# Optimization experiments

Measured on AMD Instinct MI355X. Metric: run time of the kernel, lower is better.

The kernel has to match this reference:

```python
import jax, jax.numpy as jnp
import numpy as np

PROTO_DIM = 512
PROTO_NUM = 4096
BSZ = 256
SUBTEXT_NUM = 64
TEMP = 0.9


def setup_inputs() -> dict:
    key = jax.random.key(0)
    k1, k2, k3 = jax.random.split(key, 3)
    subtexts = jax.random.normal(k1, (BSZ, SUBTEXT_NUM, PROTO_DIM), dtype=jnp.float32)
    prototype = jax.random.normal(k2, (PROTO_NUM, PROTO_DIM), dtype=jnp.float32)
    uniform = jax.random.uniform(k3, (BSZ * SUBTEXT_NUM, PROTO_NUM), dtype=jnp.float32)
    return {"subtexts": subtexts, "prototype": prototype, "uniform": uniform}


def reference(subtexts, prototype, uniform):
    # flatten: [N, D] with N = bsz * subtext_num
    flatten = subtexts.reshape(-1, PROTO_DIM)
    # dist: [N, proto_num] = flatten @ prototype.T
    dist = jnp.einsum("nd,pd->np", flatten, prototype)
    # Gumbel noise g = -log(-log(u)), matching torch F.gumbel_softmax sampling
    tiny = jnp.float32(1e-10)
    gumbel = -jnp.log(-jnp.log(uniform + tiny) + tiny)
    # noisy logits -> softmax over codebook dim (tau = curr_temp)
    soft_one_hot = jax.nn.softmax((dist + gumbel) / jnp.float32(TEMP), axis=1)
    # output: [N, D] soft codebook lookup
    output = jnp.einsum("np,pd->nd", soft_one_hot, prototype)
    proto_idx = jnp.argmax(soft_one_hot, axis=1)
    proto_loss = jnp.mean(jnp.abs(output - flatten))
    return (output, proto_loss, proto_idx)
```

## Files before the change

kernel.cpp:

```cpp
#include <hip/hip_runtime.h>
#include <math.h>

#define NROWS 16384
#define DIM   512
#define NPROTO 4096
#define TINV (1.0f / 0.9f)
#define LOSS_OFF ((size_t)NROWS * DIM)
#define IDX_OFF  ((size_t)NROWS * DIM + 1)

typedef __attribute__((ext_vector_type(8))) short short8;
typedef __attribute__((ext_vector_type(4))) float f32x4;

__global__ void zero_loss_kernel(float* out) { out[LOSS_OFF] = 0.0f; }

static __device__ __forceinline__ unsigned short f2bf(float x) {
    unsigned u = __float_as_uint(x);
    u = (u + 0x7fffu + ((u >> 16) & 1u)) >> 16;
    return (unsigned short)u;
}
static __device__ __forceinline__ float bf2f(unsigned short b) {
    return __uint_as_float(((unsigned)b) << 16);
}
static __device__ __forceinline__ void gl_lds16(const void* g, void* l) {
    __builtin_amdgcn_global_load_lds((const __attribute__((address_space(1))) unsigned int*)g,
                                     (__attribute__((address_space(3))) unsigned int*)l, 16, 0, 0);
}

__global__ __launch_bounds__(256)
void split_bf16_kernel(const float* __restrict__ src, unsigned short* __restrict__ dhi,
                       unsigned short* __restrict__ dmid, int nrows)
{
    __shared__ __align__(16) unsigned short shi[64][520];
    __shared__ __align__(16) unsigned short smid[64][520];
    const int tid = threadIdx.x;
    const int r0 = blockIdx.x * 64;
#pragma unroll
    for (int q = 0; q < 32; ++q) {
        int idx = q * 256 + tid;
        int row = idx >> 7;
        int k4 = (idx & 127) << 2;
        float4 v = *(const float4*)&src[(size_t)(r0 + row) * DIM + k4];
        unsigned short h0 = f2bf(v.x), h1 = f2bf(v.y), h2 = f2bf(v.z), h3 = f2bf(v.w);
        shi[row][k4] = h0; shi[row][k4 + 1] = h1; shi[row][k4 + 2] = h2; shi[row][k4 + 3] = h3;
        smid[row][k4]     = f2bf(v.x - bf2f(h0));
        smid[row][k4 + 1] = f2bf(v.y - bf2f(h1));
        smid[row][k4 + 2] = f2bf(v.z - bf2f(h2));
        smid[row][k4 + 3] = f2bf(v.w - bf2f(h3));
    }
    __syncthreads();
    const int row = tid & 63;
#pragma unroll
    for (int i = 0; i < 16; ++i) {
        int c = i * 4 + (tid >> 6);
        size_t o = (size_t)c * nrows + r0 + row;
        ((ulonglong2*)dhi)[o]  = *(const ulonglong2*)&shi[row][c * 8];
        ((ulonglong2*)dmid)[o] = *(const ulonglong2*)&smid[row][c * 8];
    }
}

#define BM 32
#define BN 256
#define NCHUNK (NPROTO / BN)
#define NT 16
#define CAP 80
#define PRUNE_AT 56
#define THRH 12.0f

__global__ __launch_bounds__(256, 2)
void attr_proto_mfma(const float* __restrict__ A, const float* __restrict__ Pr,
                     const float* __restrict__ U, float* __restrict__ out,
                     const unsigned short* __restrict__ wsAhi, const unsigned short* __restrict__ wsAmid,
                     const unsigned short* __restrict__ wsPhi, const unsigned short* __restrict__ wsPmid)
{
    __shared__ __align__(16) unsigned short sA[2][4][BM][8];
    __shared__ __align__(16) unsigned short sP[2][4][BN][8];
    __shared__ float hZ[BM][CAP];
    __shared__ unsigned short hI[BM][CAP];
    __shared__ int cnt[BM];
    __shared__ float mRun[BM], lRun[BM];
    __shared__ float wMax[4][BM], wSum[4][BM];
    __shared__ float epZ[8][BM];
    __shared__ int epI[8][BM];
    __shared__ int pruneFlag;

    const int tid = threadIdx.x;
    const int w = tid >> 6;
    const int lane = tid & 63;
    const int l4 = lane & 15;
    const int lh = lane >> 4;
    const int row0 = blockIdx.x * BM;

    for (int r = tid; r < BM; r += 256) { cnt[r] = 0; mRun[r] = -1e30f; lRun[r] = 0.f; }
    if (tid == 0) pruneFlag = 0;

    const unsigned short* gp[9];
    int str9[9];
    int fx9[9];
    unsigned short* ld9[9];
#pragma unroll
    for (int si = 0; si < 9; ++si) {
        int s = w * 9 + si;
        if (s < 4) {
            int sp = s >> 1, gpair = s & 1;
            int g = gpair * 2 + (lane >> 5);
            gp[si]  = (sp ? wsAmid : wsAhi) + ((size_t)g * NROWS + row0 + (lane & 31)) * 8;
            str9[si] = 4 * NROWS * 8;
            fx9[si]  = -16 * 4 * NROWS * 8;
            ld9[si] = &sA[sp][gpair * 2][0][0] + (size_t)lane * 8;
        } else {
            int p = s - 4;
            int sp = p >> 4, rem = p & 15, g = rem >> 2, q = rem & 3;
            gp[si]  = (sp ? wsPmid : wsPhi) + ((size_t)g * NPROTO + q * 64 + lane) * 8;
            str9[si] = 4 * NPROTO * 8;
            fx9[si]  = -16 * 4 * NPROTO * 8 + BN * 8;
            ld9[si] = &sP[sp][g][q * 64][0] + (size_t)lane * 8;
        }
    }
#define DO_STAGE() { _Pragma("unroll") for (int si = 0; si < 9; ++si) { gl_lds16(gp[si], ld9[si]); gp[si] += str9[si]; } }

    DO_STAGE();
    __syncthreads();

    for (int ch = 0; ch < NCHUNK; ++ch) {
        const int pbase = ch * BN;
        f32x4 acc[2][4];
#pragma unroll
        for (int mf = 0; mf < 2; ++mf)
#pragma unroll
            for (int nf = 0; nf < 4; ++nf) { acc[mf][nf][0]=0.f; acc[mf][nf][1]=0.f; acc[mf][nf][2]=0.f; acc[mf][nf][3]=0.f; }

#pragma unroll 2
        for (int t = 0; t < NT; ++t) {
            if (t > 0) {
                __syncthreads();
                DO_STAGE();
                __syncthreads();
            }
            short8 a[2][2], b[4][2];
#pragma unroll
            for (int mf = 0; mf < 2; ++mf) {
                a[mf][0] = *(const short8*)&sA[0][lh][mf * 16 + l4][0];
                a[mf][1] = *(const short8*)&sA[1][lh][mf * 16 + l4][0];
            }
#pragma unroll
            for (int nf = 0; nf < 4; ++nf) {
                b[nf][0] = *(const short8*)&sP[0][lh][w * 64 + nf * 16 + l4][0];
                b[nf][1] = *(const short8*)&sP[1][lh][w * 64 + nf * 16 + l4][0];
            }
#pragma unroll
            for (int mf = 0; mf < 2; ++mf)
#pragma unroll
                for (int nf = 0; nf < 4; ++nf) {
                    acc[mf][nf] = __builtin_amdgcn_mfma_f32_16x16x32_bf16(a[mf][0], b[nf][0], acc[mf][nf], 0, 0, 0);
                    acc[mf][nf] = __builtin_amdgcn_mfma_f32_16x16x32_bf16(a[mf][0], b[nf][1], acc[mf][nf], 0, 0, 0);
                    acc[mf][nf] = __builtin_amdgcn_mfma_f32_16x16x32_bf16(a[mf][1], b[nf][0], acc[mf][nf], 0, 0, 0);
                }
        }
        __syncthreads();
        if (ch + 1 < NCHUNK) {
#pragma unroll
            for (int si = 0; si < 9; ++si) gp[si] += fx9[si];
            DO_STAGE();
        }

#pragma unroll
        for (int mf = 0; mf < 2; ++mf) {
            float uu[16];
            const int rb = row0 + mf * 16 + lh * 4;
#pragma unroll
            for (int nf = 0; nf < 4; ++nf)
#pragma unroll
                for (int r = 0; r < 4; ++r)
                    uu[nf * 4 + r] = U[(size_t)(rb + r) * NPROTO + pbase + w * 64 + nf * 16 + l4];
#pragma unroll
            for (int nf = 0; nf < 4; ++nf)
#pragma unroll
                for (int r = 0; r < 4; ++r) {
                    float g = -__logf(-__logf(uu[nf * 4 + r] + 1e-10f) + 1e-10f);
                    acc[mf][nf][r] = (acc[mf][nf][r] + g) * TINV;
                }
        }
#pragma unroll
        for (int mf = 0; mf < 2; ++mf) {
            f32x4 rm;
#pragma unroll
            for (int r = 0; r < 4; ++r)
                rm[r] = fmaxf(fmaxf(acc[mf][0][r], acc[mf][1][r]), fmaxf(acc[mf][2][r], acc[mf][3][r]));
#pragma unroll
            for (int off = 1; off < 16; off <<= 1)
#pragma unroll
                for (int r = 0; r < 4; ++r) rm[r] = fmaxf(rm[r], __shfl_xor(rm[r], off));
            if (l4 == 0)
#pragma unroll
                for (int r = 0; r < 4; ++r) wMax[w][mf * 16 + lh * 4 + r] = rm[r];
        }
        __syncthreads();
#pragma unroll
        for (int mf = 0; mf < 2; ++mf) {
#pragma unroll
            for (int r = 0; r < 4; ++r) {
                const int rl = mf * 16 + lh * 4 + r;
                float gm = fmaxf(fmaxf(wMax[0][rl], wMax[1][rl]), fmaxf(wMax[2][rl], wMax[3][rl]));
                float mn = fmaxf(mRun[rl], gm);
                float s = 0.f;
#pragma unroll
                for (int nf = 0; nf < 4; ++nf) s += __expf(acc[mf][nf][r] - mn);
#pragma unroll
                for (int off = 1; off < 16; off <<= 1) s += __shfl_xor(s, off);
                if (l4 == 0) wSum[w][rl] = s;
                float thrv = mn - THRH;
#pragma unroll
                for (int nf = 0; nf < 4; ++nf) {
                    float z = acc[mf][nf][r];
                    if (z > thrv) {
                        int pos = atomicAdd(&cnt[rl], 1);
                        if (pos < CAP) { hZ[rl][pos] = z; hI[rl][pos] = (unsigned short)(pbase + w * 64 + nf * 16 + l4); }
                    }
                }
            }
        }
        __syncthreads();
        if (tid < BM) {
            float gm = fmaxf(fmaxf(wMax[0][tid], wMax[1][tid]), fmaxf(wMax[2][tid], wMax[3][tid]));
            float mn = fmaxf(mRun[tid], gm);
            float S = wSum[0][tid] + wSum[1][tid] + wSum[2][tid] + wSum[3][tid];
            lRun[tid] = lRun[tid] * __expf(mRun[tid] - mn) + S;
            mRun[tid] = mn;
            if (cnt[tid] > PRUNE_AT) atomicOr(&pruneFlag, 1);
        }
        __syncthreads();
        if (pruneFlag) {
            for (int r = 0; r < BM; ++r) {
                int c0 = min(cnt[r], CAP);
                if (c0 > PRUNE_AT) {
                    float thr2 = mRun[r] - THRH;
                    float ez = 0.f; int ei = 0; bool keep = false;
                    if (tid < c0) { ez = hZ[r][tid]; ei = hI[r][tid]; keep = ez > thr2; }
                    __syncthreads();
                    if (tid == 0) cnt[r] = 0;
                    __syncthreads();
                    if (keep) { int pos = atomicAdd(&cnt[r], 1); hZ[r][pos] = ez; hI[r][pos] = (unsigned short)ei; }
                    __syncthreads();
                }
            }
            if (tid == 0) pruneFlag = 0;
        }
        __syncthreads();
    }

    __syncthreads();
    const int rq = tid & 31;
    const int qq = tid >> 5;
    {
        const int c = min(cnt[rq], CAP);
        float qm = -1e30f;
        for (int e = qq; e < c; e += 8) qm = fmaxf(qm, hZ[rq][e]);
        epZ[qq][rq] = qm;
    }
    __syncthreads();
    {
        const int c = min(cnt[rq], CAP);
        float bzr = epZ[0][rq];
#pragma unroll
        for (int q = 1; q < 8; ++q) bzr = fmaxf(bzr, epZ[q][rq]);
        const float win = bzr - 3.0f;
        float bestz = -1e30f; int bestp = 1 << 30;
        const float* ap = &A[(size_t)(row0 + rq) * DIM];
        for (int e = qq; e < c; e += 8) {
            if (hZ[rq][e] > win) {
                const int p = hI[rq][e];
                const float* pp = &Pr[(size_t)p * DIM];
                float d = 0.f;
                for (int k = 0; k < DIM; k += 4) {
                    float4 av = *(const float4*)&ap[k];
                    float4 pv = *(const float4*)&pp[k];
                    d = fmaf(av.x, pv.x, d);
                    d = fmaf(av.y, pv.y, d);
                    d = fmaf(av.z, pv.z, d);
                    d = fmaf(av.w, pv.w, d);
                }
                float u = U[(size_t)(row0 + rq) * NPROTO + p];
                float g = -logf(-logf(u + 1e-10f) + 1e-10f);
                float zz = (d + g) * (1.0f / 0.9f);
                if (zz > bestz || (zz == bestz && p < bestp)) { bestz = zz; bestp = p; }
            }
        }
        __syncthreads();
        epZ[qq][rq] = bestz;
        epI[qq][rq] = bestp;
    }
    __syncthreads();
    if (tid < BM) {
        float bz2 = epZ[0][tid]; int bp2 = epI[0][tid];
#pragma unroll
        for (int q = 1; q < 8; ++q) {
            float z = epZ[q][tid]; int p = epI[q][tid];
            if (z > bz2 || (z == bz2 && p < bp2)) { bz2 = z; bp2 = p; }
        }
        out[IDX_OFF + row0 + tid] = (float)bp2;
    }

    float lossAcc = 0.f;
    for (int r = w; r < BM; r += 4) {
        const int grow = row0 + r;
        const int c = min(cnt[r], CAP);
        const float mm = mRun[r];
        const float li = 1.0f / lRun[r];
        float o[8];
#pragma unroll
        for (int q = 0; q < 8; ++q) o[q] = 0.f;
        for (int e = 0; e < c; ++e) {
            float wgt = __expf(hZ[r][e] - mm) * li;
            const float* pp = &Pr[(size_t)hI[r][e] * DIM + lane * 8];
            float4 p0 = *(const float4*)pp;
            float4 p1 = *(const float4*)(pp + 4);
            o[0] += wgt * p0.x; o[1] += wgt * p0.y; o[2] += wgt * p0.z; o[3] += wgt * p0.w;
            o[4] += wgt * p1.x; o[5] += wgt * p1.y; o[6] += wgt * p1.z; o[7] += wgt * p1.w;
        }
        const float* fr = &A[(size_t)grow * DIM + lane * 8];
        float4 f0 = *(const float4*)fr; float4 f1 = *(const float4*)(fr + 4);
        *(float4*)&out[(size_t)grow * DIM + lane * 8]     = make_float4(o[0], o[1], o[2], o[3]);
        *(float4*)&out[(size_t)grow * DIM + lane * 8 + 4] = make_float4(o[4], o[5], o[6], o[7]);
        lossAcc += fabsf(o[0] - f0.x) + fabsf(o[1] - f0.y) + fabsf(o[2] - f0.z) + fabsf(o[3] - f0.w)
                 + fabsf(o[4] - f1.x) + fabsf(o[5] - f1.y) + fabsf(o[6] - f1.z) + fabsf(o[7] - f1.w);
    }
#pragma unroll
    for (int off = 1; off < 64; off <<= 1) lossAcc += __shfl_xor(lossAcc, off);
    if (lane == 0) atomicAdd(&out[LOSS_OFF], lossAcc * (1.0f / ((float)NROWS * (float)DIM)));
}

#define FCAP 192
#define FTHR 20.0f

__global__ __launch_bounds__(256, 1)
void attr_proto_fused_valu(const float* __restrict__ A, const float* __restrict__ Pr,
                           const float* __restrict__ U, float* __restrict__ out)
{
    __shared__ __align__(16) float As[64][64 + 4];
    __shared__ __align__(16) float Bs[128][64 + 4];
    __shared__ float hZ[64][FCAP];
    __shared__ unsigned short hI[64][FCAP];
    __shared__ int cnt[64];
    __shared__ float mArr[64];
    __shared__ float lArr[64];
    __shared__ int pruneFlag;

    const int tid = threadIdx.x;
    const int tx = tid & 31;
    const int ty = tid >> 5;
    const int row0 = blockIdx.x * 64;

    for (int r = tid; r < 64; r += 256) cnt[r] = 0;
    if (tid == 0) pruneFlag = 0;

    float m[8], l[8], bz[8];
    int bi[8];
#pragma unroll
    for (int i = 0; i < 8; ++i) { m[i] = -INFINITY; l[i] = 0.0f; bz[i] = -INFINITY; bi[i] = 0; }
    __syncthreads();

    for (int ch = 0; ch < 32; ++ch) {
        const int pbase = ch * 128;
        float acc[8][4];
#pragma unroll
        for (int i = 0; i < 8; ++i)
#pragma unroll
            for (int j = 0; j < 4; ++j) acc[i][j] = 0.0f;

        for (int kk = 0; kk < DIM; kk += 64) {
#pragma unroll
            for (int q = 0; q < 4; ++q) {
                int lin = tid + q * 256;
                int lr = lin >> 4; int kq = (lin & 15) << 2;
                *(float4*)&As[lr][kq] = *(const float4*)&A[(size_t)(row0 + lr) * DIM + kk + kq];
            }
#pragma unroll
            for (int q = 0; q < 8; ++q) {
                int lin = tid + q * 256;
                int pr = lin >> 4; int kq = (lin & 15) << 2;
                *(float4*)&Bs[pr][kq] = *(const float4*)&Pr[(size_t)(pbase + pr) * DIM + kk + kq];
            }
            __syncthreads();
#pragma unroll 4
            for (int k4 = 0; k4 < 64; k4 += 4) {
                float4 av[8], bv[4];
#pragma unroll
                for (int i = 0; i < 8; ++i) av[i] = *(const float4*)&As[ty * 8 + i][k4];
#pragma unroll
                for (int j = 0; j < 4; ++j) bv[j] = *(const float4*)&Bs[tx + 32 * j][k4];
#pragma unroll
                for (int i = 0; i < 8; ++i)
#pragma unroll
                    for (int j = 0; j < 4; ++j) {
                        acc[i][j] += av[i].x * bv[j].x; acc[i][j] += av[i].y * bv[j].y;
                        acc[i][j] += av[i].z * bv[j].z; acc[i][j] += av[i].w * bv[j].w;
                    }
            }
            __syncthreads();
        }
#pragma unroll
        for (int i = 0; i < 8; ++i) {
            const int ri = ty * 8 + i;
            const size_t urow = (size_t)(row0 + ri) * NPROTO + pbase;
            float z[4]; float lmax = -INFINITY;
#pragma unroll
            for (int j = 0; j < 4; ++j) {
                float u = U[urow + tx + 32 * j];
                float g = -logf(-logf(u + 1e-10f) + 1e-10f);
                z[j] = (acc[i][j] + g) * TINV;
                lmax = fmaxf(lmax, z[j]);
            }
#pragma unroll
            for (int off = 16; off; off >>= 1) lmax = fmaxf(lmax, __shfl_xor(lmax, off, 32));
            const float mn = fmaxf(m[i], lmax);
            float s = 0.0f;
#pragma unroll
            for (int j = 0; j < 4; ++j) s += expf(z[j] - mn);
#pragma unroll
            for (int off = 16; off; off >>= 1) s += __shfl_xor(s, off, 32);
            l[i] = l[i] * expf(m[i] - mn) + s;
            m[i] = mn;
#pragma unroll
            for (int j = 0; j < 4; ++j) {
                const int p = pbase + tx + 32 * j;
                if (z[j] > bz[i]) { bz[i] = z[j]; bi[i] = p; }
                if (z[j] > mn - FTHR) {
                    int pos = atomicAdd(&cnt[ri], 1);
                    if (pos < FCAP) { hZ[ri][pos] = z[j]; hI[ri][pos] = (unsigned short)p; }
                }
            }
            if (tx == 0) {
                mArr[ri] = mn;
                if (cnt[ri] > 64) atomicOr(&pruneFlag, 1);
            }
        }
        __syncthreads();
        if (pruneFlag) {
            for (int r = 0; r < 64; ++r) {
                const int c0 = min(cnt[r], FCAP);
                if (c0 > 64) {
                    const float thr = mArr[r] - FTHR;
                    float ez = 0.0f; int ei = 0; bool keep = false;
                    if (tid < c0) { ez = hZ[r][tid]; ei = hI[r][tid]; keep = (ez > thr); }
                    __syncthreads();
                    if (tid == 0) cnt[r] = 0;
                    __syncthreads();
                    if (keep) { int pos = atomicAdd(&cnt[r], 1); hZ[r][pos] = ez; hI[r][pos] = (unsigned short)ei; }
                    __syncthreads();
                }
            }
            if (tid == 0) pruneFlag = 0;
            __syncthreads();
        }
    }
#pragma unroll
    for (int i = 0; i < 8; ++i) {
        const int ri = ty * 8 + i;
        float vz = bz[i]; int vi = bi[i];
#pragma unroll
        for (int off = 16; off; off >>= 1) {
            float oz = __shfl_xor(vz, off, 32); int oi = __shfl_xor(vi, off, 32);
            if (oz > vz || (oz == vz && oi < vi)) { vz = oz; vi = oi; }
        }
        if (tx == 0) { lArr[ri] = l[i]; out[IDX_OFF + row0 + ri] = (float)vi; }
    }
    __syncthreads();

    const int wv = tid >> 6;
    const int lane = tid & 63;
    float lossAcc = 0.0f;
    for (int r = wv; r < 64; r += 4) {
        const int grow = row0 + r;
        const int c = min(cnt[r], FCAP);
        const float mm = mArr[r];
        const float li = 1.0f / lArr[r];
        float o[8];
#pragma unroll
        for (int q = 0; q < 8; ++q) o[q] = 0.0f;
        for (int e = 0; e < c; ++e) {
            const float wg = expf(hZ[r][e] - mm) * li;
            const float* pp = &Pr[(size_t)hI[r][e] * DIM + lane * 8];
            float4 p0 = *(const float4*)pp; float4 p1 = *(const float4*)(pp + 4);
            o[0] += wg * p0.x; o[1] += wg * p0.y; o[2] += wg * p0.z; o[3] += wg * p0.w;
            o[4] += wg * p1.x; o[5] += wg * p1.y; o[6] += wg * p1.z; o[7] += wg * p1.w;
        }
        const float* fr = &A[(size_t)grow * DIM + lane * 8];
        float4 f0 = *(const float4*)fr; float4 f1 = *(const float4*)(fr + 4);
        *(float4*)&out[(size_t)grow * DIM + lane * 8]     = make_float4(o[0], o[1], o[2], o[3]);
        *(float4*)&out[(size_t)grow * DIM + lane * 8 + 4] = make_float4(o[4], o[5], o[6], o[7]);
        lossAcc += fabsf(o[0]-f0.x) + fabsf(o[1]-f0.y) + fabsf(o[2]-f0.z) + fabsf(o[3]-f0.w)
                 + fabsf(o[4]-f1.x) + fabsf(o[5]-f1.y) + fabsf(o[6]-f1.z) + fabsf(o[7]-f1.w);
    }
#pragma unroll
    for (int off = 32; off; off >>= 1) lossAcc += __shfl_xor(lossAcc, off, 64);
    if (lane == 0) atomicAdd(&out[LOSS_OFF], lossAcc * (1.0f / ((float)NROWS * (float)DIM)));
}

extern "C" void kernel_launch(void* const* d_in, const int* in_sizes, int n_in,
                              void* d_out, int out_size, void* d_ws, size_t ws_size,
                              hipStream_t stream)
{
    const float* A  = (const float*)d_in[0];
    const float* Pr = (const float*)d_in[1];
    const float* U  = (const float*)d_in[2];
    float* out = (float*)d_out;

    const size_t NA = (size_t)NROWS * DIM;
    const size_t NP = (size_t)NPROTO * DIM;
    const size_t need = (2 * NA + 2 * NP) * sizeof(unsigned short);

    if (ws_size >= need) {
        unsigned short* wsAhi  = (unsigned short*)d_ws;
        unsigned short* wsAmid = wsAhi + NA;
        unsigned short* wsPhi  = wsAmid + NA;
        unsigned short* wsPmid = wsPhi + NP;
        split_bf16_kernel<<<NROWS / 64, 256, 0, stream>>>(A, wsAhi, wsAmid, NROWS);
        split_bf16_kernel<<<NPROTO / 64, 256, 0, stream>>>(Pr, wsPhi, wsPmid, NPROTO);
        zero_loss_kernel<<<1, 1, 0, stream>>>(out);
        attr_proto_mfma<<<NROWS / BM, 256, 0, stream>>>(A, Pr, U, out, wsAhi, wsAmid, wsPhi, wsPmid);
    } else {
        zero_loss_kernel<<<1, 1, 0, stream>>>(out);
        attr_proto_fused_valu<<<NROWS / 64, 256, 0, stream>>>(A, Pr, U, out);
    }
}
```

Measured before the change: 478.0 us.

## Split fused kernel into double-buffered GEMM-collect and per-row finish kernels

```diff
diff --git a/kernel.cpp b/kernel.cpp
--- a/kernel.cpp
+++ b/kernel.cpp
@@ -7,6 +7,8 @@
 #define TINV (1.0f / 0.9f)
 #define LOSS_OFF ((size_t)NROWS * DIM)
 #define IDX_OFF  ((size_t)NROWS * DIM + 1)
+#define LCAP 128
+#define LTHR 10.0f
 
 typedef __attribute__((ext_vector_type(8))) short short8;
 typedef __attribute__((ext_vector_type(4))) float f32x4;
@@ -62,20 +64,270 @@
 #define BN 256
 #define NCHUNK (NPROTO / BN)
 #define NT 16
-#define CAP 80
-#define PRUNE_AT 56
-#define THRH 12.0f
 
 __global__ __launch_bounds__(256, 2)
-void attr_proto_mfma(const float* __restrict__ A, const float* __restrict__ Pr,
-                     const float* __restrict__ U, float* __restrict__ out,
-                     const unsigned short* __restrict__ wsAhi, const unsigned short* __restrict__ wsAmid,
-                     const unsigned short* __restrict__ wsPhi, const unsigned short* __restrict__ wsPmid)
+void gemm_collect(const float* __restrict__ U,
+                  int* __restrict__ gCnt, uint2* __restrict__ gList,
+                  const unsigned short* __restrict__ wsAhi, const unsigned short* __restrict__ wsAmid,
+                  const unsigned short* __restrict__ wsPhi, const unsigned short* __restrict__ wsPmid)
+{
+    __shared__ __align__(16) unsigned short sA[2][2][4][BM][8];
+    __shared__ __align__(16) unsigned short sP[2][2][4][BN][8];
+    __shared__ float wMax[4][BM];
+    __shared__ float mRun[BM];
+
+    const int tid = threadIdx.x;
+    const int w = tid >> 6;
+    const int lane = tid & 63;
+    const int l4 = lane & 15;
+    const int lh = lane >> 4;
+    const int row0 = blockIdx.x * BM;
+
+    if (tid < BM) mRun[tid] = -1e30f;
+
+    const unsigned short* gp[9];
+    int str9[9], fx9[9], bstr9[9];
+    unsigned short* ld9[9];
+#pragma unroll
+    for (int si = 0; si < 9; ++si) {
+        int s = w * 9 + si;
+        if (s < 4) {
+            int sp = s >> 1, gpair = s & 1;
+            int g = gpair * 2 + (lane >> 5);
+            gp[si]  = (sp ? wsAmid : wsAhi) + ((size_t)g * NROWS + row0 + (lane & 31)) * 8;
+            str9[si] = 4 * NROWS * 8;
+            fx9[si]  = -16 * 4 * NROWS * 8;
+            ld9[si]  = &sA[0][sp][gpair * 2][0][0] + (size_t)lane * 8;
+            bstr9[si] = 2 * 4 * BM * 8;
+        } else {
+            int p = s - 4;
+            int sp = p >> 4, rem = p & 15, g = rem >> 2, q = rem & 3;
+            gp[si]  = (sp ? wsPmid : wsPhi) + ((size_t)g * NPROTO + q * 64 + lane) * 8;
+            str9[si] = 4 * NPROTO * 8;
+            fx9[si]  = -16 * 4 * NPROTO * 8 + BN * 8;
+            ld9[si]  = &sP[0][sp][g][q * 64][0] + (size_t)lane * 8;
+            bstr9[si] = 2 * 4 * BN * 8;
+        }
+    }
+#define DO_STAGE(b) { _Pragma("unroll") for (int si = 0; si < 9; ++si) { \
+        gl_lds16(gp[si], ld9[si] + ((b) ? bstr9[si] : 0)); gp[si] += str9[si]; } }
+
+    DO_STAGE(0);
+    __syncthreads();
+
+    for (int ch = 0; ch < NCHUNK; ++ch) {
+        const int pbase = ch * BN;
+        f32x4 acc[2][4];
+#pragma unroll
+        for (int mf = 0; mf < 2; ++mf)
+#pragma unroll
+            for (int nf = 0; nf < 4; ++nf) { acc[mf][nf][0]=0.f; acc[mf][nf][1]=0.f; acc[mf][nf][2]=0.f; acc[mf][nf][3]=0.f; }
+
+#pragma unroll 2
+        for (int t = 0; t < NT; ++t) {
+            const int cur = t & 1;
+            if (t < NT - 1) {
+                DO_STAGE(cur ^ 1);
+            } else if (ch + 1 < NCHUNK) {
+#pragma unroll
+                for (int si = 0; si < 9; ++si) gp[si] += fx9[si];
+                DO_STAGE(cur ^ 1);
+            }
+            short8 a[2][2], b[4][2];
+#pragma unroll
+            for (int mf = 0; mf < 2; ++mf) {
+                a[mf][0] = *(const short8*)&sA[cur][0][lh][mf * 16 + l4][0];
+                a[mf][1] = *(const short8*)&sA[cur][1][lh][mf * 16 + l4][0];
+            }
+#pragma unroll
+            for (int nf = 0; nf < 4; ++nf) {
+                b[nf][0] = *(const short8*)&sP[cur][0][lh][w * 64 + nf * 16 + l4][0];
+                b[nf][1] = *(const short8*)&sP[cur][1][lh][w * 64 + nf * 16 + l4][0];
+            }
+#pragma unroll
+            for (int mf = 0; mf < 2; ++mf)
+#pragma unroll
+                for (int nf = 0; nf < 4; ++nf) {
+                    acc[mf][nf] = __builtin_amdgcn_mfma_f32_16x16x32_bf16(a[mf][0], b[nf][0], acc[mf][nf], 0, 0, 0);
+                    acc[mf][nf] = __builtin_amdgcn_mfma_f32_16x16x32_bf16(a[mf][0], b[nf][1], acc[mf][nf], 0, 0, 0);
+                    acc[mf][nf] = __builtin_amdgcn_mfma_f32_16x16x32_bf16(a[mf][1], b[nf][0], acc[mf][nf], 0, 0, 0);
+                }
+            __syncthreads();
+        }
+
+#pragma unroll
+        for (int mf = 0; mf < 2; ++mf) {
+            float uu[16];
+            const int rb = row0 + mf * 16 + lh * 4;
+#pragma unroll
+            for (int nf = 0; nf < 4; ++nf)
+#pragma unroll
+                for (int r = 0; r < 4; ++r)
+                    uu[nf * 4 + r] = U[(size_t)(rb + r) * NPROTO + pbase + w * 64 + nf * 16 + l4];
+#pragma unroll
+            for (int nf = 0; nf < 4; ++nf)
+#pragma unroll
+                for (int r = 0; r < 4; ++r) {
+                    float g = -__logf(-__logf(uu[nf * 4 + r] + 1e-10f) + 1e-10f);
+                    acc[mf][nf][r] = (acc[mf][nf][r] + g) * TINV;
+                }
+        }
+#pragma unroll
+        for (int mf = 0; mf < 2; ++mf) {
+            f32x4 rm;
+#pragma unroll
+            for (int r = 0; r < 4; ++r)
+                rm[r] = fmaxf(fmaxf(acc[mf][0][r], acc[mf][1][r]), fmaxf(acc[mf][2][r], acc[mf][3][r]));
+#pragma unroll
+            for (int off = 1; off < 16; off <<= 1)
+#pragma unroll
+                for (int r = 0; r < 4; ++r) rm[r] = fmaxf(rm[r], __shfl_xor(rm[r], off));
+            if (l4 == 0)
+#pragma unroll
+                for (int r = 0; r < 4; ++r) wMax[w][mf * 16 + lh * 4 + r] = rm[r];
+        }
+        __syncthreads();
+#pragma unroll
+        for (int mf = 0; mf < 2; ++mf) {
+#pragma unroll
+            for (int r = 0; r < 4; ++r) {
+                const int rl = mf * 16 + lh * 4 + r;
+                float gm = fmaxf(fmaxf(wMax[0][rl], wMax[1][rl]), fmaxf(wMax[2][rl], wMax[3][rl]));
+                float mn = fmaxf(mRun[rl], gm);
+                float thrv = mn - LTHR;
+#pragma unroll
+                for (int nf = 0; nf < 4; ++nf) {
+                    float z = acc[mf][nf][r];
+                    if (z > thrv) {
+                        int pos = atomicAdd(&gCnt[row0 + rl], 1);
+                        if (pos < LCAP) {
+                            uint2 en; en.x = __float_as_uint(z); en.y = (unsigned)(pbase + w * 64 + nf * 16 + l4);
+                            gList[(size_t)(row0 + rl) * LCAP + pos] = en;
+                        }
+                    }
+                }
+            }
+        }
+        __syncthreads();
+        if (tid < BM) {
+            float gm = fmaxf(fmaxf(wMax[0][tid], wMax[1][tid]), fmaxf(wMax[2][tid], wMax[3][tid]));
+            mRun[tid] = fmaxf(mRun[tid], gm);
+        }
+    }
+#undef DO_STAGE
+}
+
+__global__ __launch_bounds__(256)
+void finish_kernel(const float* __restrict__ A, const float* __restrict__ Pr,
+                   const float* __restrict__ U, float* __restrict__ out,
+                   const int* __restrict__ gCnt, const uint2* __restrict__ gList,
+                   float* __restrict__ wsLoss)
+{
+    const int tid = threadIdx.x;
+    const int lane = tid & 63;
+    const int row = blockIdx.x * 4 + (tid >> 6);
+    const int c = min(gCnt[row], LCAP);
+    const uint2* lst = &gList[(size_t)row * LCAP];
+
+    float M = -1e30f;
+    for (int e = lane; e < c; e += 64) M = fmaxf(M, __uint_as_float(lst[e].x));
+#pragma unroll
+    for (int off = 1; off < 64; off <<= 1) M = fmaxf(M, __shfl_xor(M, off));
+    const float cutoff = M - LTHR;
+
+    float L = 0.f, bz = -1e30f; int bi = 1 << 30;
+    for (int e = lane; e < c; e += 64) {
+        float z = __uint_as_float(lst[e].x); int p = (int)lst[e].y;
+        if (z > cutoff) {
+            L += __expf(z - M);
+            if (z > bz || (z == bz && p < bi)) { bz = z; bi = p; }
+        }
+    }
+#pragma unroll
+    for (int off = 1; off < 64; off <<= 1) {
+        L += __shfl_xor(L, off);
+        float oz = __shfl_xor(bz, off); int oi = __shfl_xor(bi, off);
+        if (oz > bz || (oz == bz && oi < bi)) { bz = oz; bi = oi; }
+    }
+
+    float bestz = -1e30f; int bestp = 1 << 30;
+    const float* ap = &A[(size_t)row * DIM];
+    for (int e = lane; e < c; e += 64) {
+        float z = __uint_as_float(lst[e].x);
+        if (z > bz - 3.0f) {
+            int p = (int)lst[e].y;
+            const float* pp = &Pr[(size_t)p * DIM];
+            float d = 0.f;
+            for (int k = 0; k < DIM; k += 4) {
+                float4 av = *(const float4*)&ap[k];
+                float4 pv = *(const float4*)&pp[k];
+                d = fmaf(av.x, pv.x, d);
+                d = fmaf(av.y, pv.y, d);
+                d = fmaf(av.z, pv.z, d);
+                d = fmaf(av.w, pv.w, d);
+            }
+            float u = U[(size_t)row * NPROTO + p];
+            float g = -logf(-logf(u + 1e-10f) + 1e-10f);
+            float zz = (d + g) * (1.0f / 0.9f);
+            if (zz > bestz || (zz == bestz && p < bestp)) { bestz = zz; bestp = p; }
+        }
+    }
+#pragma unroll
+    for (int off = 1; off < 64; off <<= 1) {
+        float oz = __shfl_xor(bestz, off); int oi = __shfl_xor(bestp, off);
+        if (oz > bestz || (oz == bestz && oi < bestp)) { bestz = oz; bestp = oi; }
+    }
+    if (lane == 0) out[IDX_OFF + row] = (float)bestp;
+
+    float o[8];
+#pragma unroll
+    for (int q = 0; q < 8; ++q) o[q] = 0.f;
+    const float Li = 1.0f / L;
+    for (int e = 0; e < c; ++e) {
+        uint2 en = lst[e];
+        float z = __uint_as_float(en.x);
+        if (z > cutoff) {
+            float wgt = __expf(z - M) * Li;
+            const float* pp = &Pr[(size_t)en.y * DIM + lane * 8];
+            float4 p0 = *(const float4*)pp;
+            float4 p1 = *(const float4*)(pp + 4);
+            o[0] += wgt * p0.x; o[1] += wgt * p0.y; o[2] += wgt * p0.z; o[3] += wgt * p0.w;
+            o[4] += wgt * p1.x; o[5] += wgt * p1.y; o[6] += wgt * p1.z; o[7] += wgt * p1.w;
+        }
+    }
+    const float* fr = &A[(size_t)row * DIM + lane * 8];
+    float4 f0 = *(const float4*)fr; float4 f1 = *(const float4*)(fr + 4);
+    *(float4*)&out[(size_t)row * DIM + lane * 8]     = make_float4(o[0], o[1], o[2], o[3]);
+    *(float4*)&out[(size_t)row * DIM + lane * 8 + 4] = make_float4(o[4], o[5], o[6], o[7]);
+    float lossAcc = fabsf(o[0]-f0.x) + fabsf(o[1]-f0.y) + fabsf(o[2]-f0.z) + fabsf(o[3]-f0.w)
+                  + fabsf(o[4]-f1.x) + fabsf(o[5]-f1.y) + fabsf(o[6]-f1.z) + fabsf(o[7]-f1.w);
+#pragma unroll
+    for (int off = 1; off < 64; off <<= 1) lossAcc += __shfl_xor(lossAcc, off);
+    if (lane == 0) atomicAdd(&wsLoss[blockIdx.x & 63], lossAcc * (1.0f / ((float)NROWS * (float)DIM)));
+}
+
+__global__ void loss_final_kernel(const float* __restrict__ wsLoss, float* __restrict__ out)
+{
+    float s = wsLoss[threadIdx.x];
+#pragma unroll
+    for (int off = 1; off < 64; off <<= 1) s += __shfl_xor(s, off);
+    if (threadIdx.x == 0) out[LOSS_OFF] = s;
+}
+
+#define FCAP 80
+#define FPRUNE_AT 56
+#define FTHRH 12.0f
+
+__global__ __launch_bounds__(256, 2)
+void attr_proto_mfma_fb(const float* __restrict__ A, const float* __restrict__ Pr,
+                        const float* __restrict__ U, float* __restrict__ out,
+                        const unsigned short* __restrict__ wsAhi, const unsigned short* __restrict__ wsAmid,
+                        const unsigned short* __restrict__ wsPhi, const unsigned short* __restrict__ wsPmid)
 {
     __shared__ __align__(16) unsigned short sA[2][4][BM][8];
     __shared__ __align__(16) unsigned short sP[2][4][BN][8];
-    __shared__ float hZ[BM][CAP];
-    __shared__ unsigned short hI[BM][CAP];
+    __shared__ float hZ[BM][FCAP];
+    __shared__ unsigned short hI[BM][FCAP];
     __shared__ int cnt[BM];
     __shared__ float mRun[BM], lRun[BM];
     __shared__ float wMax[4][BM], wSum[4][BM];
@@ -116,9 +368,9 @@
             ld9[si] = &sP[sp][g][q * 64][0] + (size_t)lane * 8;
         }
     }
-#define DO_STAGE() { _Pragma("unroll") for (int si = 0; si < 9; ++si) { gl_lds16(gp[si], ld9[si]); gp[si] += str9[si]; } }
-
-    DO_STAGE();
+#define FB_STAGE() { _Pragma("unroll") for (int si = 0; si < 9; ++si) { gl_lds16(gp[si], ld9[si]); gp[si] += str9[si]; } }
+
+    FB_STAGE();
     __syncthreads();
 
     for (int ch = 0; ch < NCHUNK; ++ch) {
@@ -133,7 +385,7 @@
         for (int t = 0; t < NT; ++t) {
             if (t > 0) {
                 __syncthreads();
-                DO_STAGE();
+                FB_STAGE();
                 __syncthreads();
             }
             short8 a[2][2], b[4][2];
@@ -160,7 +412,7 @@
         if (ch + 1 < NCHUNK) {
 #pragma unroll
             for (int si = 0; si < 9; ++si) gp[si] += fx9[si];
-            DO_STAGE();
+            FB_STAGE();
         }
 
 #pragma unroll
@@ -208,13 +460,13 @@
 #pragma unroll
                 for (int off = 1; off < 16; off <<= 1) s += __shfl_xor(s, off);
                 if (l4 == 0) wSum[w][rl] = s;
-                float thrv = mn - THRH;
+                float thrv = mn - FTHRH;
 #pragma unroll
                 for (int nf = 0; nf < 4; ++nf) {
                     float z = acc[mf][nf][r];
                     if (z > thrv) {
                         int pos = atomicAdd(&cnt[rl], 1);
-                        if (pos < CAP) { hZ[rl][pos] = z; hI[rl][pos] = (unsigned short)(pbase + w * 64 + nf * 16 + l4); }
+                        if (pos < FCAP) { hZ[rl][pos] = z; hI[rl][pos] = (unsigned short)(pbase + w * 64 + nf * 16 + l4); }
                     }
                 }
             }
@@ -226,14 +478,14 @@
             float S = wSum[0][tid] + wSum[1][tid] + wSum[2][tid] + wSum[3][tid];
             lRun[tid] = lRun[tid] * __expf(mRun[tid] - mn) + S;
             mRun[tid] = mn;
-            if (cnt[tid] > PRUNE_AT) atomicOr(&pruneFlag, 1);
+            if (cnt[tid] > FPRUNE_AT) atomicOr(&pruneFlag, 1);
         }
         __syncthreads();
         if (pruneFlag) {
             for (int r = 0; r < BM; ++r) {
-                int c0 = min(cnt[r], CAP);
-                if (c0 > PRUNE_AT) {
-                    float thr2 = mRun[r] - THRH;
+                int c0 = min(cnt[r], FCAP);
+                if (c0 > FPRUNE_AT) {
+                    float thr2 = mRun[r] - FTHRH;
                     float ez = 0.f; int ei = 0; bool keep = false;
                     if (tid < c0) { ez = hZ[r][tid]; ei = hI[r][tid]; keep = ez > thr2; }
                     __syncthreads();
@@ -252,14 +504,14 @@
     const int rq = tid & 31;
     const int qq = tid >> 5;
     {
-        const int c = min(cnt[rq], CAP);
+        const int c = min(cnt[rq], FCAP);
         float qm = -1e30f;
         for (int e = qq; e < c; e += 8) qm = fmaxf(qm, hZ[rq][e]);
         epZ[qq][rq] = qm;
     }
     __syncthreads();
     {
-        const int c = min(cnt[rq], CAP);
+        const int c = min(cnt[rq], FCAP);
         float bzr = epZ[0][rq];
 #pragma unroll
         for (int q = 1; q < 8; ++q) bzr = fmaxf(bzr, epZ[q][rq]);
@@ -303,7 +555,7 @@
     float lossAcc = 0.f;
     for (int r = w; r < BM; r += 4) {
         const int grow = row0 + r;
-        const int c = min(cnt[r], CAP);
+        const int c = min(cnt[r], FCAP);
         const float mm = mRun[r];
         const float li = 1.0f / lRun[r];
         float o[8];
@@ -327,173 +579,7 @@
 #pragma unroll
     for (int off = 1; off < 64; off <<= 1) lossAcc += __shfl_xor(lossAcc, off);
     if (lane == 0) atomicAdd(&out[LOSS_OFF], lossAcc * (1.0f / ((float)NROWS * (float)DIM)));
-}
-
-#define FCAP 192
-#define FTHR 20.0f
-
-__global__ __launch_bounds__(256, 1)
-void attr_proto_fused_valu(const float* __restrict__ A, const float* __restrict__ Pr,
-                           const float* __restrict__ U, float* __restrict__ out)
-{
-    __shared__ __align__(16) float As[64][64 + 4];
-    __shared__ __align__(16) float Bs[128][64 + 4];
-    __shared__ float hZ[64][FCAP];
-    __shared__ unsigned short hI[64][FCAP];
-    __shared__ int cnt[64];
-    __shared__ float mArr[64];
-    __shared__ float lArr[64];
-    __shared__ int pruneFlag;
-
-    const int tid = threadIdx.x;
-    const int tx = tid & 31;
-    const int ty = tid >> 5;
-    const int row0 = blockIdx.x * 64;
-
-    for (int r = tid; r < 64; r += 256) cnt[r] = 0;
-    if (tid == 0) pruneFlag = 0;
-
-    float m[8], l[8], bz[8];
-    int bi[8];
-#pragma unroll
-    for (int i = 0; i < 8; ++i) { m[i] = -INFINITY; l[i] = 0.0f; bz[i] = -INFINITY; bi[i] = 0; }
-    __syncthreads();
-
-    for (int ch = 0; ch < 32; ++ch) {
-        const int pbase = ch * 128;
-        float acc[8][4];
-#pragma unroll
-        for (int i = 0; i < 8; ++i)
-#pragma unroll
-            for (int j = 0; j < 4; ++j) acc[i][j] = 0.0f;
-
-        for (int kk = 0; kk < DIM; kk += 64) {
-#pragma unroll
-            for (int q = 0; q < 4; ++q) {
-                int lin = tid + q * 256;
-                int lr = lin >> 4; int kq = (lin & 15) << 2;
-                *(float4*)&As[lr][kq] = *(const float4*)&A[(size_t)(row0 + lr) * DIM + kk + kq];
-            }
-#pragma unroll
-            for (int q = 0; q < 8; ++q) {
-                int lin = tid + q * 256;
-                int pr = lin >> 4; int kq = (lin & 15) << 2;
-                *(float4*)&Bs[pr][kq] = *(const float4*)&Pr[(size_t)(pbase + pr) * DIM + kk + kq];
-            }
-            __syncthreads();
-#pragma unroll 4
-            for (int k4 = 0; k4 < 64; k4 += 4) {
-                float4 av[8], bv[4];
-#pragma unroll
-                for (int i = 0; i < 8; ++i) av[i] = *(const float4*)&As[ty * 8 + i][k4];
-#pragma unroll
-                for (int j = 0; j < 4; ++j) bv[j] = *(const float4*)&Bs[tx + 32 * j][k4];
-#pragma unroll
-                for (int i = 0; i < 8; ++i)
-#pragma unroll
-                    for (int j = 0; j < 4; ++j) {
-                        acc[i][j] += av[i].x * bv[j].x; acc[i][j] += av[i].y * bv[j].y;
-                        acc[i][j] += av[i].z * bv[j].z; acc[i][j] += av[i].w * bv[j].w;
-                    }
-            }
-            __syncthreads();
-        }
-#pragma unroll
-        for (int i = 0; i < 8; ++i) {
-            const int ri = ty * 8 + i;
-            const size_t urow = (size_t)(row0 + ri) * NPROTO + pbase;
-            float z[4]; float lmax = -INFINITY;
-#pragma unroll
-            for (int j = 0; j < 4; ++j) {
-                float u = U[urow + tx + 32 * j];
-                float g = -logf(-logf(u + 1e-10f) + 1e-10f);
-                z[j] = (acc[i][j] + g) * TINV;
-                lmax = fmaxf(lmax, z[j]);
-            }
-#pragma unroll
-            for (int off = 16; off; off >>= 1) lmax = fmaxf(lmax, __shfl_xor(lmax, off, 32));
-            const float mn = fmaxf(m[i], lmax);
-            float s = 0.0f;
-#pragma unroll
-            for (int j = 0; j < 4; ++j) s += expf(z[j] - mn);
-#pragma unroll
-            for (int off = 16; off; off >>= 1) s += __shfl_xor(s, off, 32);
-            l[i] = l[i] * expf(m[i] - mn) + s;
-            m[i] = mn;
-#pragma unroll
-            for (int j = 0; j < 4; ++j) {
-                const int p = pbase + tx + 32 * j;
-                if (z[j] > bz[i]) { bz[i] = z[j]; bi[i] = p; }
-                if (z[j] > mn - FTHR) {
-                    int pos = atomicAdd(&cnt[ri], 1);
-                    if (pos < FCAP) { hZ[ri][pos] = z[j]; hI[ri][pos] = (unsigned short)p; }
-                }
-            }
-            if (tx == 0) {
-                mArr[ri] = mn;
-                if (cnt[ri] > 64) atomicOr(&pruneFlag, 1);
-            }
-        }
-        __syncthreads();
-        if (pruneFlag) {
-            for (int r = 0; r < 64; ++r) {
-                const int c0 = min(cnt[r], FCAP);
-                if (c0 > 64) {
-                    const float thr = mArr[r] - FTHR;
-                    float ez = 0.0f; int ei = 0; bool keep = false;
-                    if (tid < c0) { ez = hZ[r][tid]; ei = hI[r][tid]; keep = (ez > thr); }
-                    __syncthreads();
-                    if (tid == 0) cnt[r] = 0;
-                    __syncthreads();
-                    if (keep) { int pos = atomicAdd(&cnt[r], 1); hZ[r][pos] = ez; hI[r][pos] = (unsigned short)ei; }
-                    __syncthreads();
-                }
-            }
-            if (tid == 0) pruneFlag = 0;
-            __syncthreads();
-        }
-    }
-#pragma unroll
-    for (int i = 0; i < 8; ++i) {
-        const int ri = ty * 8 + i;
-        float vz = bz[i]; int vi = bi[i];
-#pragma unroll
-        for (int off = 16; off; off >>= 1) {
-            float oz = __shfl_xor(vz, off, 32); int oi = __shfl_xor(vi, off, 32);
-            if (oz > vz || (oz == vz && oi < vi)) { vz = oz; vi = oi; }
-        }
-        if (tx == 0) { lArr[ri] = l[i]; out[IDX_OFF + row0 + ri] = (float)vi; }
-    }
-    __syncthreads();
-
-    const int wv = tid >> 6;
-    const int lane = tid & 63;
-    float lossAcc = 0.0f;
-    for (int r = wv; r < 64; r += 4) {
-        const int grow = row0 + r;
-        const int c = min(cnt[r], FCAP);
-        const float mm = mArr[r];
-        const float li = 1.0f / lArr[r];
-        float o[8];
-#pragma unroll
-        for (int q = 0; q < 8; ++q) o[q] = 0.0f;
-        for (int e = 0; e < c; ++e) {
-            const float wg = expf(hZ[r][e] - mm) * li;
-            const float* pp = &Pr[(size_t)hI[r][e] * DIM + lane * 8];
-            float4 p0 = *(const float4*)pp; float4 p1 = *(const float4*)(pp + 4);
-            o[0] += wg * p0.x; o[1] += wg * p0.y; o[2] += wg * p0.z; o[3] += wg * p0.w;
-            o[4] += wg * p1.x; o[5] += wg * p1.y; o[6] += wg * p1.z; o[7] += wg * p1.w;
-        }
-        const float* fr = &A[(size_t)grow * DIM + lane * 8];
-        float4 f0 = *(const float4*)fr; float4 f1 = *(const float4*)(fr + 4);
-        *(float4*)&out[(size_t)grow * DIM + lane * 8]     = make_float4(o[0], o[1], o[2], o[3]);
-        *(float4*)&out[(size_t)grow * DIM + lane * 8 + 4] = make_float4(o[4], o[5], o[6], o[7]);
-        lossAcc += fabsf(o[0]-f0.x) + fabsf(o[1]-f0.y) + fabsf(o[2]-f0.z) + fabsf(o[3]-f0.w)
-                 + fabsf(o[4]-f1.x) + fabsf(o[5]-f1.y) + fabsf(o[6]-f1.z) + fabsf(o[7]-f1.w);
-    }
-#pragma unroll
-    for (int off = 32; off; off >>= 1) lossAcc += __shfl_xor(lossAcc, off, 64);
-    if (lane == 0) atomicAdd(&out[LOSS_OFF], lossAcc * (1.0f / ((float)NROWS * (float)DIM)));
+#undef FB_STAGE
 }
 
 extern "C" void kernel_launch(void* const* d_in, const int* in_sizes, int n_in,
@@ -507,19 +593,30 @@
 
     const size_t NA = (size_t)NROWS * DIM;
     const size_t NP = (size_t)NPROTO * DIM;
-    const size_t need = (2 * NA + 2 * NP) * sizeof(unsigned short);
-
-    if (ws_size >= need) {
-        unsigned short* wsAhi  = (unsigned short*)d_ws;
-        unsigned short* wsAmid = wsAhi + NA;
-        unsigned short* wsPhi  = wsAmid + NA;
-        unsigned short* wsPmid = wsPhi + NP;
-        split_bf16_kernel<<<NROWS / 64, 256, 0, stream>>>(A, wsAhi, wsAmid, NROWS);
-        split_bf16_kernel<<<NPROTO / 64, 256, 0, stream>>>(Pr, wsPhi, wsPmid, NPROTO);
-        zero_loss_kernel<<<1, 1, 0, stream>>>(out);
-        attr_proto_mfma<<<NROWS / BM, 256, 0, stream>>>(A, Pr, U, out, wsAhi, wsAmid, wsPhi, wsPmid);
+    const size_t splitBytes = (2 * NA + 2 * NP) * sizeof(unsigned short);
+    const size_t cntBytes   = (size_t)NROWS * sizeof(int);
+    const size_t lossBytes  = 64 * sizeof(float);
+    const size_t listBytes  = (size_t)NROWS * LCAP * sizeof(uint2);
+    const size_t needSplit  = splitBytes + cntBytes + lossBytes + listBytes;
+
+    unsigned short* wsAhi  = (unsigned short*)d_ws;
+    unsigned short* wsAmid = wsAhi + NA;
+    unsigned short* wsPhi  = wsAmid + NA;
+    unsigned short* wsPmid = wsPhi + NP;
+
+    split_bf16_kernel<<<NROWS / 64, 256, 0, stream>>>(A, wsAhi, wsAmid, NROWS);
+    split_bf16_kernel<<<NPROTO / 64, 256, 0, stream>>>(Pr, wsPhi, wsPmid, NPROTO);
+
+    if (ws_size >= needSplit) {
+        int*   gCnt   = (int*)((char*)d_ws + splitBytes);
+        float* wsLoss = (float*)((char*)d_ws + splitBytes + cntBytes);
+        uint2* gList  = (uint2*)((char*)d_ws + splitBytes + cntBytes + lossBytes);
+        hipMemsetAsync(gCnt, 0, cntBytes + lossBytes, stream);
+        gemm_collect<<<NROWS / BM, 256, 0, stream>>>(U, gCnt, gList, wsAhi, wsAmid, wsPhi, wsPmid);
+        finish_kernel<<<NROWS / 4, 256, 0, stream>>>(A, Pr, U, out, gCnt, gList, wsLoss);
+        loss_final_kernel<<<1, 64, 0, stream>>>(wsLoss, out);
     } else {
         zero_loss_kernel<<<1, 1, 0, stream>>>(out);
-        attr_proto_fused_valu<<<NROWS / 64, 256, 0, stream>>>(A, Pr, U, out);
-    }
-}
+        attr_proto_mfma_fb<<<NROWS / BM, 256, 0, stream>>>(A, Pr, U, out, wsAhi, wsAmid, wsPhi, wsPmid);
+    }
+}
```

Measured after the change: 528.0 us. 10.5% more time.
